# Optimization experiments

Measured on AMD Instinct MI355X. Metric: run time of the kernel, lower is better.

Reference implementation:

```python
import jax, jax.numpy as jnp
import numpy as np

NUM_SCOPES, NUM_DECOMPS, BATCH, NUM_IN, NUM_SUMS = 32, 8, 256, 256, 256


def setup_inputs() -> dict:
    key = jax.random.key(0)
    k1, k2 = jax.random.split(key)
    # x: log-probabilities from children, shape [scopes, decomps, batch, num_nodes_in]
    x = jax.random.normal(k1, (NUM_SCOPES, NUM_DECOMPS, BATCH, NUM_IN), dtype=jnp.float32)
    # accumulators: positive weights, shape [scopes, decomps, num_nodes_in, num_sums]
    accumulators = jax.random.uniform(
        k2, (NUM_SCOPES, NUM_DECOMPS, NUM_IN, NUM_SUMS), dtype=jnp.float32,
        minval=1e-3, maxval=1.0)
    return {"x": x, "accumulators": accumulators}


def _logmatmul(x, logw):
    # out[s,d,b,j] = logsumexp_i( x[s,d,b,i] + logw[s,d,i,j] )
    # Stable form: factor out per-row / per-col maxes, do a real GEMM in linear space.
    xmax = jnp.max(x, axis=3, keepdims=True)            # [s,d,b,1]
    wmax = jnp.max(logw, axis=2, keepdims=True)         # [s,d,1,j]
    y = jnp.einsum('sdbi,sdij->sdbj', jnp.exp(x - xmax), jnp.exp(logw - wmax))
    return jnp.log(y) + xmax + wmax                     # [s,d,b,j]


def reference(x, accumulators):
    # Default path: logspace_accumulators=False, backprop_mode=GRADIENT
    log_weights = jax.nn.log_softmax(jnp.log(accumulators), axis=2)
    return _logmatmul(x, log_weights)
```

## Files before the change

kernel.cpp:

```cpp
#include <hip/hip_runtime.h>


#define NB  256
#define NI  256
#define NJ  256

typedef __attribute__((ext_vector_type(8))) short bf16x8;
typedef __attribute__((ext_vector_type(4))) float f32x4;

__device__ __forceinline__ unsigned short f2bf(float f) {
  unsigned int u = __float_as_uint(f);
  u += 0x7FFFu + ((u >> 16) & 1u);
  return (unsigned short)(u >> 16);
}

__global__ __launch_bounds__(512, 2)
void densesum_kernel(const float* __restrict__ x,
                     const float* __restrict__ acc,
                     float* __restrict__ out) {
  const int sd = blockIdx.x;
  const float* xb = x   + (size_t)sd * NB * NI;
  const float* ab = acc + (size_t)sd * NI * NJ;
  float*       ob = out + (size_t)sd * NB * NJ;

  __shared__ unsigned short As[NB * 64];
  __shared__ unsigned short Bs[NJ * 64];
  __shared__ float colpart[8 * NJ];
  __shared__ float logS[NJ];

  const int tid  = threadIdx.x;
  const int lane = tid & 63;
  const int wid  = tid >> 6;
  const int wr   = wid >> 2;
  const int wc   = wid & 3;
  const int l15  = lane & 15;
  const int lk   = lane >> 4;
  const int r    = (lane >> 1) & 3;
  const bool s1 = (r & 1), s2 = (r & 2);

  f32x4 C[8][4];
  #pragma unroll
  for (int m = 0; m < 8; ++m)
    #pragma unroll
    for (int n = 0; n < 4; ++n)
      C[m][n] = (f32x4){0.f, 0.f, 0.f, 0.f};

  float bsum0 = 0.f, bsum1 = 0.f, bsum2 = 0.f, bsum3 = 0.f;

  float4 pa[8];
  float4 pb[8];

  auto loadA = [&](int kc) {
    #pragma unroll
    for (int it = 0; it < 8; ++it) {
      int q  = tid + it * 512;
      int b  = q >> 4;
      int c0 = (q & 15) * 4;
      pa[it] = *reinterpret_cast<const float4*>(xb + (size_t)b * NI + kc * 64 + c0);
    }
  };
  auto loadB = [&](int kc) {
    #pragma unroll
    for (int t = 0; t < 2; ++t) {
      int q  = tid + t * 512;
      int kl = (q >> 6) * 4;
      int jb = (q & 63) * 4;
      const float* src = ab + (size_t)(kc * 64 + kl) * NJ + jb;
      pb[t * 4 + 0] = *reinterpret_cast<const float4*>(src);
      pb[t * 4 + 1] = *reinterpret_cast<const float4*>(src + NJ);
      pb[t * 4 + 2] = *reinterpret_cast<const float4*>(src + 2 * NJ);
      pb[t * 4 + 3] = *reinterpret_cast<const float4*>(src + 3 * NJ);
    }
  };
  auto convA = [&]() {
    #pragma unroll
    for (int it = 0; it < 8; ++it) {
      int q  = tid + it * 512;
      int b  = q >> 4;
      int c0 = (q & 15) * 4;
      ushort4 h;
      h.x = f2bf(__expf(pa[it].x));
      h.y = f2bf(__expf(pa[it].y));
      h.z = f2bf(__expf(pa[it].z));
      h.w = f2bf(__expf(pa[it].w));
      *reinterpret_cast<ushort4*>(&As[b * 64 + (c0 ^ ((b & 7) << 3))]) = h;
    }
  };
  auto convB = [&]() {
    #pragma unroll
    for (int t = 0; t < 2; ++t) {
      int q  = tid + t * 512;
      int kl = (q >> 6) * 4;
      int jb = (q & 63) * 4;
      float4 v0 = pb[t * 4 + 0], v1 = pb[t * 4 + 1];
      float4 v2 = pb[t * 4 + 2], v3 = pb[t * 4 + 3];
      #define ROT(v, u0, u1, u2, u3)                                            \
        { float t0 = s1 ? v.y : v.x, t1 = s1 ? v.z : v.y,                       \
                t2 = s1 ? v.w : v.z, t3 = s1 ? v.x : v.w;                       \
          u0 = s2 ? t2 : t0; u1 = s2 ? t3 : t1;                                 \
          u2 = s2 ? t0 : t2; u3 = s2 ? t1 : t3; }
      float a00, a01, a02, a03; ROT(v0, a00, a01, a02, a03);
      float a10, a11, a12, a13; ROT(v1, a10, a11, a12, a13);
      float a20, a21, a22, a23; ROT(v2, a20, a21, a22, a23);
      float a30, a31, a32, a33; ROT(v3, a30, a31, a32, a33);
      #undef ROT
      #define STORE_COL(cc, w0, w1, w2, w3)                                     \
        { int jc = jb + ((cc + r) & 3);                                         \
          bsum##cc += w0 + w1 + w2 + w3;                                        \
          ushort4 h; h.x = f2bf(w0); h.y = f2bf(w1);                            \
          h.z = f2bf(w2); h.w = f2bf(w3);                                       \
          *reinterpret_cast<ushort4*>(&Bs[jc * 64 + (kl ^ ((jc & 7) << 3))]) = h; }
      STORE_COL(0, a00, a10, a20, a30);
      STORE_COL(1, a01, a11, a21, a31);
      STORE_COL(2, a02, a12, a22, a32);
      STORE_COL(3, a03, a13, a23, a33);
      #undef STORE_COL
    }
  };

  loadA(0);
  loadB(0);
  for (int kc = 0; kc < 4; ++kc) {
    convA();
    convB();
    __syncthreads();
    if (kc < 3) {
      loadA(kc + 1);
      loadB(kc + 1);
    }
    #pragma unroll
    for (int ks = 0; ks < 2; ++ks) {
      const int k0 = ks * 32 + 8 * lk;
      bf16x8 bfr[4];
      #pragma unroll
      for (int n = 0; n < 4; ++n) {
        int row = wc * 64 + n * 16 + l15;
        bfr[n] = *reinterpret_cast<const bf16x8*>(&Bs[row * 64 + (k0 ^ ((row & 7) << 3))]);
      }
      #pragma unroll
      for (int m = 0; m < 8; ++m) {
        int row = wr * 128 + m * 16 + l15;
        bf16x8 af = *reinterpret_cast<const bf16x8*>(&As[row * 64 + (k0 ^ ((row & 7) << 3))]);
        #pragma unroll
        for (int n = 0; n < 4; ++n)
          C[m][n] = __builtin_amdgcn_mfma_f32_16x16x32_bf16(af, bfr[n], C[m][n], 0, 0, 0);
      }
    }
    __syncthreads();
  }

  {
    int jb = lane * 4;
    colpart[wid * NJ + jb + ((0 + r) & 3)] = bsum0;
    colpart[wid * NJ + jb + ((1 + r) & 3)] = bsum1;
    colpart[wid * NJ + jb + ((2 + r) & 3)] = bsum2;
    colpart[wid * NJ + jb + ((3 + r) & 3)] = bsum3;
  }
  __syncthreads();
  if (tid < NJ) {
    float s = 0.f;
    #pragma unroll
    for (int c = 0; c < 8; ++c) s += colpart[c * NJ + tid];
    logS[tid] = __logf(s);
  }
  __syncthreads();

  #pragma unroll
  for (int m = 0; m < 8; ++m) {
    int b0 = wr * 128 + m * 16 + lk * 4;
    #pragma unroll
    for (int n = 0; n < 4; ++n) {
      int j = wc * 64 + n * 16 + l15;
      float ls = logS[j];
      #pragma unroll
      for (int rr = 0; rr < 4; ++rr) {
        ob[(size_t)(b0 + rr) * NJ + j] = __logf(C[m][n][rr]) - ls;
      }
    }
  }
}

extern "C" void kernel_launch(void* const* d_in, const int* in_sizes, int n_in,
                              void* d_out, int out_size, void* d_ws, size_t ws_size,
                              hipStream_t stream) {
  const float* x   = (const float*)d_in[0];
  const float* acc = (const float*)d_in[1];
  float* out = (float*)d_out;
  hipLaunchKernelGGL(densesum_kernel, dim3(256), dim3(512), 0, stream, x, acc, out);
}
```

Baseline: 41.70 us.

## Split batch into two halves and keep full bf16 weight matrix in LDS

```diff
diff --git a/kernel.cpp b/kernel.cpp
--- a/kernel.cpp
+++ b/kernel.cpp
@@ -4,6 +4,7 @@
 #define NB  256
 #define NI  256
 #define NJ  256
+#define BH  128
 
 typedef __attribute__((ext_vector_type(8))) short bf16x8;
 typedef __attribute__((ext_vector_type(4))) float f32x4;
@@ -23,8 +24,8 @@
   const float* ab = acc + (size_t)sd * NI * NJ;
   float*       ob = out + (size_t)sd * NB * NJ;
 
-  __shared__ unsigned short As[NB * 64];
-  __shared__ unsigned short Bs[NJ * 64];
+  __shared__ unsigned short As[BH * 64];
+  __shared__ unsigned short Bs[NJ * NI];
   __shared__ float colpart[8 * NJ];
   __shared__ float logS[NJ];
 
@@ -38,25 +39,26 @@
   const int r    = (lane >> 1) & 3;
   const bool s1 = (r & 1), s2 = (r & 2);
 
-  f32x4 C[8][4];
-  #pragma unroll
-  for (int m = 0; m < 8; ++m)
-    #pragma unroll
-    for (int n = 0; n < 4; ++n)
-      C[m][n] = (f32x4){0.f, 0.f, 0.f, 0.f};
-
+  f32x4 C[4][4];
   float bsum0 = 0.f, bsum1 = 0.f, bsum2 = 0.f, bsum3 = 0.f;
-
-  float4 pa[8];
+  float4 pa[4];
   float4 pb[8];
 
-  auto loadA = [&](int kc) {
-    #pragma unroll
-    for (int it = 0; it < 8; ++it) {
+  auto zeroC = [&]() {
+    #pragma unroll
+    for (int m = 0; m < 4; ++m)
+      #pragma unroll
+      for (int n = 0; n < 4; ++n)
+        C[m][n] = (f32x4){0.f, 0.f, 0.f, 0.f};
+  };
+
+  auto loadA = [&](const float* xh, int kc) {
+    #pragma unroll
+    for (int it = 0; it < 4; ++it) {
       int q  = tid + it * 512;
       int b  = q >> 4;
       int c0 = (q & 15) * 4;
-      pa[it] = *reinterpret_cast<const float4*>(xb + (size_t)b * NI + kc * 64 + c0);
+      pa[it] = *reinterpret_cast<const float4*>(xh + (size_t)b * NI + kc * 64 + c0);
     }
   };
   auto loadB = [&](int kc) {
@@ -74,7 +76,7 @@
   };
   auto convA = [&]() {
     #pragma unroll
-    for (int it = 0; it < 8; ++it) {
+    for (int it = 0; it < 4; ++it) {
       int q  = tid + it * 512;
       int b  = q >> 4;
       int c0 = (q & 15) * 4;
@@ -86,12 +88,13 @@
       *reinterpret_cast<ushort4*>(&As[b * 64 + (c0 ^ ((b & 7) << 3))]) = h;
     }
   };
-  auto convB = [&]() {
+  auto convB = [&](int kc) {
     #pragma unroll
     for (int t = 0; t < 2; ++t) {
-      int q  = tid + t * 512;
-      int kl = (q >> 6) * 4;
-      int jb = (q & 63) * 4;
+      int q   = tid + t * 512;
+      int kl  = (q >> 6) * 4;
+      int jb  = (q & 63) * 4;
+      int kg  = kc * 64 + kl;
       float4 v0 = pb[t * 4 + 0], v1 = pb[t * 4 + 1];
       float4 v2 = pb[t * 4 + 2], v3 = pb[t * 4 + 3];
       #define ROT(v, u0, u1, u2, u3)                                            \
@@ -109,7 +112,7 @@
           bsum##cc += w0 + w1 + w2 + w3;                                        \
           ushort4 h; h.x = f2bf(w0); h.y = f2bf(w1);                            \
           h.z = f2bf(w2); h.w = f2bf(w3);                                       \
-          *reinterpret_cast<ushort4*>(&Bs[jc * 64 + (kl ^ ((jc & 7) << 3))]) = h; }
+          *reinterpret_cast<ushort4*>(&Bs[jc * NI + (kg ^ ((jc & 7) << 3))]) = h; }
       STORE_COL(0, a00, a10, a20, a30);
       STORE_COL(1, a01, a11, a21, a31);
       STORE_COL(2, a02, a12, a22, a32);
@@ -117,35 +120,58 @@
       #undef STORE_COL
     }
   };
-
-  loadA(0);
-  loadB(0);
-  for (int kc = 0; kc < 4; ++kc) {
-    convA();
-    convB();
-    __syncthreads();
-    if (kc < 3) {
-      loadA(kc + 1);
-      loadB(kc + 1);
-    }
+  auto mfmaChunk = [&](int kc) {
     #pragma unroll
     for (int ks = 0; ks < 2; ++ks) {
-      const int k0 = ks * 32 + 8 * lk;
+      const int ka = ks * 32 + 8 * lk;
+      const int kg = kc * 64 + ka;
       bf16x8 bfr[4];
       #pragma unroll
       for (int n = 0; n < 4; ++n) {
         int row = wc * 64 + n * 16 + l15;
-        bfr[n] = *reinterpret_cast<const bf16x8*>(&Bs[row * 64 + (k0 ^ ((row & 7) << 3))]);
+        bfr[n] = *reinterpret_cast<const bf16x8*>(&Bs[row * NI + (kg ^ ((row & 7) << 3))]);
       }
       #pragma unroll
-      for (int m = 0; m < 8; ++m) {
-        int row = wr * 128 + m * 16 + l15;
-        bf16x8 af = *reinterpret_cast<const bf16x8*>(&As[row * 64 + (k0 ^ ((row & 7) << 3))]);
+      for (int m = 0; m < 4; ++m) {
+        int row = wr * 64 + m * 16 + l15;
+        bf16x8 af = *reinterpret_cast<const bf16x8*>(&As[row * 64 + (ka ^ ((row & 7) << 3))]);
         #pragma unroll
         for (int n = 0; n < 4; ++n)
           C[m][n] = __builtin_amdgcn_mfma_f32_16x16x32_bf16(af, bfr[n], C[m][n], 0, 0, 0);
       }
     }
+  };
+  auto epilogue = [&](int bh) {
+    float* obh = ob + (size_t)bh * BH * NJ;
+    #pragma unroll
+    for (int m = 0; m < 4; ++m) {
+      int b0 = wr * 64 + m * 16 + lk * 4;
+      #pragma unroll
+      for (int n = 0; n < 4; ++n) {
+        int j = wc * 64 + n * 16 + l15;
+        float ls = logS[j];
+        #pragma unroll
+        for (int rr = 0; rr < 4; ++rr) {
+          obh[(size_t)(b0 + rr) * NJ + j] = __logf(C[m][n][rr]) - ls;
+        }
+      }
+    }
+  };
+
+  loadA(xb, 0);
+  loadB(0);
+  zeroC();
+  for (int kc = 0; kc < 4; ++kc) {
+    convA();
+    convB(kc);
+    __syncthreads();
+    if (kc < 3) {
+      loadA(xb, kc + 1);
+      loadB(kc + 1);
+    } else {
+      loadA(xb + (size_t)BH * NI, 0);
+    }
+    mfmaChunk(kc);
     __syncthreads();
   }
 
@@ -165,19 +191,18 @@
   }
   __syncthreads();
 
-  #pragma unroll
-  for (int m = 0; m < 8; ++m) {
-    int b0 = wr * 128 + m * 16 + lk * 4;
-    #pragma unroll
-    for (int n = 0; n < 4; ++n) {
-      int j = wc * 64 + n * 16 + l15;
-      float ls = logS[j];
-      #pragma unroll
-      for (int rr = 0; rr < 4; ++rr) {
-        ob[(size_t)(b0 + rr) * NJ + j] = __logf(C[m][n][rr]) - ls;
-      }
-    }
-  }
+  epilogue(0);
+
+  zeroC();
+  for (int kc = 0; kc < 4; ++kc) {
+    convA();
+    __syncthreads();
+    if (kc < 3) loadA(xb + (size_t)BH * NI, kc + 1);
+    mfmaChunk(kc);
+    __syncthreads();
+  }
+
+  epilogue(1);
 }
 
 extern "C" void kernel_launch(void* const* d_in, const int* in_sizes, int n_in,
```

Result: faster. 38.25 us (-8.3%).
